# Kernel optimization log

Measured on AMD Instinct MI355X. Metric: run time of the kernel, lower is better.

The kernel has to match this reference:

```python
import jax, jax.numpy as jnp
import numpy as np

B, N, K = 32, 4096, 8          # batch, num input features (64x64 map), num slots
HID, D, DM = 256, 256, 512     # hid_dim, slot_dim, mlp_hid_dim
ITERS = 3
TEMP = 1.0
EPS = 1e-8
SCALE = D ** -0.5              # (slot_dim // num_heads) ** -0.5, heads=1


def layer_norm(x, g, b):
    m = jnp.mean(x, axis=-1, keepdims=True)
    v = jnp.mean((x - m) ** 2, axis=-1, keepdims=True)
    return (x - m) * jax.lax.rsqrt(v + 1e-5) * g + b


def setup_inputs() -> dict:
    key = jax.random.key(0)
    ks = jax.random.split(key, 20)
    s = 0.02
    inp = {
        "inputs": jax.random.normal(ks[0], (B, N, HID), jnp.float32),
        "noise": jax.random.normal(ks[1], (B, K, D), jnp.float32),
        "slots_mu": jax.random.normal(ks[2], (1, 1, D), jnp.float32),
        "slots_sigma": jnp.abs(jax.random.normal(ks[3], (1, 1, D), jnp.float32)),
        "ln_in_g": jnp.ones((HID,), jnp.float32),
        "ln_in_b": jnp.zeros((HID,), jnp.float32),
        "ln_slots_g": jnp.ones((D,), jnp.float32),
        "ln_slots_b": jnp.zeros((D,), jnp.float32),
        "ln_mlp_g": jnp.ones((D,), jnp.float32),
        "ln_mlp_b": jnp.zeros((D,), jnp.float32),
        # Linear weights stored [in, out]
        "Wq": jax.random.normal(ks[4], (D, D), jnp.float32) * s,
        "bq": jnp.zeros((D,), jnp.float32),
        "Wk": jax.random.normal(ks[5], (HID, D), jnp.float32) * s,
        "bk": jnp.zeros((D,), jnp.float32),
        "Wv": jax.random.normal(ks[6], (HID, D), jnp.float32) * s,
        "bv": jnp.zeros((D,), jnp.float32),
        # GRUCell params (torch layout transposed to [in, 3D])
        "W_ih": jax.random.normal(ks[7], (D, 3 * D), jnp.float32) * s,
        "W_hh": jax.random.normal(ks[8], (D, 3 * D), jnp.float32) * s,
        "b_ih": jnp.zeros((3 * D,), jnp.float32),
        "b_hh": jnp.zeros((3 * D,), jnp.float32),
        # residual MLP
        "W1": jax.random.normal(ks[9], (D, DM), jnp.float32) * s,
        "b1": jnp.zeros((DM,), jnp.float32),
        "W2": jax.random.normal(ks[10], (DM, D), jnp.float32) * s,
        "b2": jnp.zeros((D,), jnp.float32),
    }
    return inp


def reference(inputs, noise, slots_mu, slots_sigma,
              ln_in_g, ln_in_b, ln_slots_g, ln_slots_b, ln_mlp_g, ln_mlp_b,
              Wq, bq, Wk, bk, Wv, bv,
              W_ih, W_hh, b_ih, b_hh,
              W1, b1, W2, b2):
    x = layer_norm(inputs, ln_in_g, ln_in_b)            # [B,N,HID]
    k = x @ Wk + bk                                     # [B,N,D]
    v = x @ Wv + bv                                     # [B,N,D]

    slots = slots_mu + slots_sigma * noise              # [B,K,D]

    for _ in range(ITERS):
        slots_prev = slots
        s = layer_norm(slots, ln_slots_g, ln_slots_b)
        q = s @ Wq + bq                                  # [B,K,D]
        dots = jnp.einsum('bkd,bnd->bkn', q, k) * SCALE / TEMP
        attn = jax.nn.softmax(dots, axis=1)              # inverted: over slot axis
        attn = attn + EPS
        attn = attn / jnp.sum(attn, axis=2, keepdims=True)  # weighted mean over keys
        updates = jnp.einsum('bkn,bnd->bkd', attn, v)    # [B,K,D]

        # GRUCell on flattened (B*K, D)
        xg = updates.reshape(-1, D)
        h = slots_prev.reshape(-1, D)
        gi = xg @ W_ih + b_ih
        gh = h @ W_hh + b_hh
        i_r, i_z, i_n = jnp.split(gi, 3, axis=-1)
        h_r, h_z, h_n = jnp.split(gh, 3, axis=-1)
        r = jax.nn.sigmoid(i_r + h_r)
        z = jax.nn.sigmoid(i_z + h_z)
        n = jnp.tanh(i_n + r * h_n)
        h = (1.0 - z) * n + z * h
        slots = h.reshape(B, K, D)

        # residual MLP
        m = layer_norm(slots, ln_mlp_g, ln_mlp_b)
        slots = slots + (jax.nn.relu(m @ W1 + b1) @ W2 + b2)

    return slots
```

## Files before the change

kernel.cpp:

```cpp
#include <hip/hip_runtime.h>
#include <hip/hip_bf16.h>

#define NB 32
#define NPOS 4096
#define NSLOT 8
#define HIDD 256
#define DDIM 256
#define SCALE_F 0.0625f
#define EPS_F 1e-8f
#define NCHUNK 32
#define CPOS 128
#define TPOS 32

typedef __attribute__((ext_vector_type(4))) float f32x4;
typedef __attribute__((ext_vector_type(8))) short s16x8;
typedef __attribute__((ext_vector_type(2))) unsigned int u32x2;
typedef _Float16 h16x2 __attribute__((ext_vector_type(2)));

__device__ __forceinline__ unsigned short f2bf(float f) {
    unsigned int x = __float_as_uint(f);
    x = (x + 0x7fffu + ((x >> 16) & 1u)) >> 16;
    return (unsigned short)x;
}
__device__ __forceinline__ unsigned short f2h(float f) {
    _Float16 h = (_Float16)f;
    return __builtin_bit_cast(unsigned short, h);
}
__device__ __forceinline__ h16x2 u2h(unsigned u) { return __builtin_bit_cast(h16x2, u); }
__device__ __forceinline__ h16x2 mkh(float a0, float a1) {
    h16x2 r; r[0] = (_Float16)a0; r[1] = (_Float16)a1; return r;
}
__device__ __forceinline__ void dot4(f32x4& acc, uint4 wv, h16x2 av) {
    acc[0] = __builtin_amdgcn_fdot2(av, u2h(wv.x), acc[0], false);
    acc[1] = __builtin_amdgcn_fdot2(av, u2h(wv.y), acc[1], false);
    acc[2] = __builtin_amdgcn_fdot2(av, u2h(wv.z), acc[2], false);
    acc[3] = __builtin_amdgcn_fdot2(av, u2h(wv.w), acc[3], false);
}

__global__ __launch_bounds__(256) void k_ln_in(
        const float* __restrict__ x, const float* __restrict__ g,
        const float* __restrict__ b, unsigned short* __restrict__ lnx) {
    int lane = threadIdx.x & 63;
    int wave = threadIdx.x >> 6;
    long row = (long)blockIdx.x * 4 + wave;
    const float4* xr = (const float4*)(x + row * 256);
    float4 v = xr[lane];
    float s = v.x + v.y + v.z + v.w;
    float sq = v.x * v.x + v.y * v.y + v.z * v.z + v.w * v.w;
    #pragma unroll
    for (int m = 32; m; m >>= 1) { s += __shfl_xor(s, m); sq += __shfl_xor(sq, m); }
    float mean = s * 0.00390625f;
    float rstd = rsqrtf(sq * 0.00390625f - mean * mean + 1e-5f);
    const float4 gg = ((const float4*)g)[lane];
    const float4 bb = ((const float4*)b)[lane];
    ushort4 o;
    o.x = f2bf((v.x - mean) * rstd * gg.x + bb.x);
    o.y = f2bf((v.y - mean) * rstd * gg.y + bb.y);
    o.z = f2bf((v.z - mean) * rstd * gg.z + bb.z);
    o.w = f2bf((v.w - mean) * rstd * gg.w + bb.w);
    ((ushort4*)(lnx + row * 256))[lane] = o;
}

__device__ __forceinline__ unsigned packrowh(const float* __restrict__ W, int hp, int N, int c) {
    return (unsigned)f2h(W[(2*hp)*N + c]) | ((unsigned)f2h(W[(2*hp+1)*N + c]) << 16);
}

__global__ __launch_bounds__(256) void k_prep(
        const float* __restrict__ Wq, const float* __restrict__ Wk,
        const float* __restrict__ Wv, const float* __restrict__ Wih,
        const float* __restrict__ Whh, const float* __restrict__ W1,
        const float* __restrict__ W2,
        unsigned* __restrict__ WqP, unsigned* __restrict__ WkTP,
        unsigned* __restrict__ WvP, unsigned* __restrict__ WihP,
        unsigned* __restrict__ WhhP, unsigned* __restrict__ W1P,
        unsigned* __restrict__ W2P) {
    int i = blockIdx.x * 256 + threadIdx.x;
    if (i < 32768) {
        int hp = i >> 8, c = i & 255;
        WqP[i] = packrowh(Wq, hp, 256, c);
        WvP[i] = packrowh(Wv, hp, 256, c);
        WkTP[i] = (unsigned)f2h(Wk[c*256 + 2*hp]) | ((unsigned)f2h(Wk[c*256 + 2*hp + 1]) << 16);
    }
    if (i < 65536) {
        int hp1 = i >> 9, c1 = i & 511;
        W1P[i] = packrowh(W1, hp1, 512, c1);
        int hp2 = i >> 8, c2 = i & 255;
        W2P[i] = packrowh(W2, hp2, 256, c2);
    }
    if (i < 98304) {
        int hp = i / 768, c = i % 768;
        WihP[i] = packrowh(Wih, hp, 768, c);
        WhhP[i] = packrowh(Whh, hp, 768, c);
    }
}

__device__ __forceinline__ void qk_tail(
        float v0, float v1, int b, int s0,
        const float* __restrict__ lng, const float* __restrict__ lnb,
        const float* __restrict__ Wq, const float* __restrict__ bq,
        const float* __restrict__ Wk, const float* __restrict__ bk,
        unsigned short* __restrict__ qkg, float* __restrict__ qbkg,
        float (*sh)[256], float (*red)[4]) {
    int c = threadIdx.x;
    float s_0 = v0, q_0 = v0 * v0, s_1 = v1, q_1 = v1 * v1;
    #pragma unroll
    for (int m = 32; m; m >>= 1) {
        s_0 += __shfl_xor(s_0, m); q_0 += __shfl_xor(q_0, m);
        s_1 += __shfl_xor(s_1, m); q_1 += __shfl_xor(q_1, m);
    }
    if ((c & 63) == 0) { int w = c >> 6; red[w][0]=s_0; red[w][1]=q_0; red[w][2]=s_1; red[w][3]=q_1; }
    __syncthreads();
    float S0 = red[0][0]+red[1][0]+red[2][0]+red[3][0];
    float Q0 = red[0][1]+red[1][1]+red[2][1]+red[3][1];
    float S1 = red[0][2]+red[1][2]+red[2][2]+red[3][2];
    float Q1 = red[0][3]+red[1][3]+red[2][3]+red[3][3];
    float m0 = S0 * 0.00390625f, r0 = rsqrtf(Q0 * 0.00390625f - m0*m0 + 1e-5f);
    float m1 = S1 * 0.00390625f, r1 = rsqrtf(Q1 * 0.00390625f - m1*m1 + 1e-5f);
    float gc = lng[c], bc = lnb[c];
    sh[0][c] = (v0 - m0) * r0 * gc + bc;
    sh[1][c] = (v1 - m1) * r1 * gc + bc;
    __syncthreads();
    float qa0 = bq[c], qa1 = qa0;
    for (int h = 0; h < 256; h += 4) {
        float w0 = Wq[(h+0)*256+c], w1 = Wq[(h+1)*256+c];
        float w2 = Wq[(h+2)*256+c], w3 = Wq[(h+3)*256+c];
        float4 x0 = *(const float4*)&sh[0][h], x1 = *(const float4*)&sh[1][h];
        qa0 += x0.x*w0 + x0.y*w1 + x0.z*w2 + x0.w*w3;
        qa1 += x1.x*w0 + x1.y*w1 + x1.z*w2 + x1.w*w3;
    }
    __syncthreads();
    sh[0][c] = qa0; sh[1][c] = qa1;
    float bkc = bk[c];
    float p0 = qa0 * bkc, p1 = qa1 * bkc;
    #pragma unroll
    for (int m = 32; m; m >>= 1) { p0 += __shfl_xor(p0, m); p1 += __shfl_xor(p1, m); }
    __syncthreads();
    if ((c & 63) == 0) { int w = c >> 6; red[w][0] = p0; red[w][1] = p1; }
    __syncthreads();
    if (c < 2) qbkg[b*8 + s0 + c] = SCALE_F * (red[0][c]+red[1][c]+red[2][c]+red[3][c]);
    float k0 = 0.f, k1 = 0.f;
    const float* wkr = Wk + (long)c * 256;
    for (int d = 0; d < 256; d += 4) {
        float4 wk4 = *(const float4*)&wkr[d];
        float4 x0 = *(const float4*)&sh[0][d], x1 = *(const float4*)&sh[1][d];
        k0 += x0.x*wk4.x + x0.y*wk4.y + x0.z*wk4.z + x0.w*wk4.w;
        k1 += x1.x*wk4.x + x1.y*wk4.y + x1.z*wk4.z + x1.w*wk4.w;
    }
    qkg[(b*8 + s0    )*256 + c] = f2bf(SCALE_F * k0);
    qkg[(b*8 + s0 + 1)*256 + c] = f2bf(SCALE_F * k1);
}

__global__ __launch_bounds__(256) void k_init(
        const float* __restrict__ noise, const float* __restrict__ mu,
        const float* __restrict__ sig, const float* __restrict__ lng,
        const float* __restrict__ lnb, const float* __restrict__ Wq,
        const float* __restrict__ bq, const float* __restrict__ Wk,
        const float* __restrict__ bk, float* __restrict__ slots,
        unsigned short* __restrict__ qkg, float* __restrict__ qbkg) {
    __shared__ float sh[2][256];
    __shared__ float red[4][4];
    int b = blockIdx.x >> 2, rp = blockIdx.x & 3;
    int s0 = rp * 2, r0 = b * 8 + s0;
    int c = threadIdx.x;
    float v0 = mu[c] + sig[c] * noise[r0*256 + c];
    float v1 = mu[c] + sig[c] * noise[(r0+1)*256 + c];
    slots[r0*256 + c] = v0;
    slots[(r0+1)*256 + c] = v1;
    qk_tail(v0, v1, b, s0, lng, lnb, Wq, bq, Wk, bk, qkg, qbkg, sh, red);
}

__global__ __launch_bounds__(128) void k_stream(
        const unsigned short* __restrict__ lnx, const unsigned short* __restrict__ qk,
        const float* __restrict__ qbk, float* __restrict__ Upart,
        float* __restrict__ dpart) {
    __shared__ unsigned short xt[TPOS * 256];
    __shared__ float Ured[8 * 256];
    __shared__ float dred[8];
    int b = blockIdx.x >> 5, ch = blockIdx.x & 31;
    int t = threadIdx.x;
    int l = t & 63, w = t >> 6;
    for (int i = t; i < 2048; i += 128) Ured[i] = 0.f;
    if (t < 8) dred[t] = 0.f;
    int slot = l & 15, g = l >> 4;
    s16x8 qkf[8];
    float qbkv = 0.f;
    if (slot < 8) {
        const unsigned short* qrow = qk + (b*8 + slot) * 256;
        #pragma unroll
        for (int hk = 0; hk < 8; hk++)
            qkf[hk] = *(const s16x8*)(qrow + hk*32 + 8*g);
        qbkv = qbk[b*8 + slot];
    } else {
        #pragma unroll
        for (int hk = 0; hk < 8; hk++) qkf[hk] = (s16x8)0;
    }
    f32x4 uacc[16];
    #pragma unroll
    for (int i = 0; i < 16; i++) uacc[i] = (f32x4)0.f;
    float dreg = 0.f;
    int gbase = (b * NPOS + ch * CPOS) * 256;
    int pw = w * 16;
    __syncthreads();
    for (int tile = 0; tile < 4; tile++) {
        #pragma unroll
        for (int i = 0; i < 8; i++) {
            int c = t + 128 * i;
            int p = c >> 5, hc = c & 31;
            int4 v = *(const int4*)(lnx + gbase + (tile*TPOS + p)*256 + hc*8);
            *(int4*)&xt[p*256 + ((hc ^ (p & 15)) << 3)] = v;
        }
        __syncthreads();
        f32x4 acc = (f32x4)0.f;
        {
            int prow = pw + (l & 15);
            const unsigned short* xrow = &xt[prow * 256];
            int sw = prow & 15;
            #pragma unroll
            for (int hk = 0; hk < 8; hk++) {
                s16x8 a = *(const s16x8*)(xrow + (((hk*4 + g) ^ sw) << 3));
                acc = __builtin_amdgcn_mfma_f32_16x16x32_bf16(a, qkf[hk], acc, 0, 0, 0);
            }
        }
        float at[4];
        #pragma unroll
        for (int r = 0; r < 4; r++) {
            float v = acc[r] + qbkv;
            float m = v;
            m = fmaxf(m, __shfl_xor(m, 1));
            m = fmaxf(m, __shfl_xor(m, 2));
            m = fmaxf(m, __shfl_xor(m, 4));
            float e = __expf(v - m);
            float sum = e;
            sum += __shfl_xor(sum, 1);
            sum += __shfl_xor(sum, 2);
            sum += __shfl_xor(sum, 4);
            float a = e / sum;
            at[r] = a;
            dreg += a;
        }
        u32x2 a2;
        a2.x = (unsigned)f2bf(at[0]) | ((unsigned)f2bf(at[1]) << 16);
        a2.y = (unsigned)f2bf(at[2]) | ((unsigned)f2bf(at[3]) << 16);
        int p0 = pw + 4 * g;
        int hl = l & 7;
        #pragma unroll
        for (int hc = 0; hc < 16; hc++) {
            int hcol = hc * 2 + ((l & 15) >> 3);
            unsigned e0 = xt[(p0+0)*256 + ((hcol ^ ((p0+0) & 15)) << 3) + hl];
            unsigned e1 = xt[(p0+1)*256 + ((hcol ^ ((p0+1) & 15)) << 3) + hl];
            unsigned e2 = xt[(p0+2)*256 + ((hcol ^ ((p0+2) & 15)) << 3) + hl];
            unsigned e3 = xt[(p0+3)*256 + ((hcol ^ ((p0+3) & 15)) << 3) + hl];
            u32x2 b2;
            b2.x = e0 | (e1 << 16);
            b2.y = e2 | (e3 << 16);
            asm volatile("v_mfma_f32_16x16x16_bf16 %0, %1, %2, %0"
                         : "+v"(uacc[hc]) : "v"(a2), "v"(b2));
        }
        __syncthreads();
    }
    if (g < 2) {
        #pragma unroll
        for (int hc = 0; hc < 16; hc++) {
            int h = hc * 16 + (l & 15);
            #pragma unroll
            for (int r = 0; r < 4; r++)
                atomicAdd(&Ured[(4*g + r)*256 + h], uacc[hc][r]);
        }
    }
    dreg += __shfl_xor(dreg, 16);
    dreg += __shfl_xor(dreg, 32);
    if (slot < 8 && g == 0) atomicAdd(&dred[slot], dreg);
    __syncthreads();
    float* up = Upart + (long)(b * NCHUNK + ch) * 2048;
    for (int i = t; i < 2048; i += 128) up[i] = Ured[i];
    if (t < 8) dpart[(b * NCHUNK + ch) * 8 + t] = dred[t];
}

__device__ __forceinline__ float ln1024(float v, int c, const float* __restrict__ g,
                                        const float* __restrict__ b, float (*red)[2]) {
    float s1 = v, s2 = v * v;
    #pragma unroll
    for (int m = 32; m; m >>= 1) { s1 += __shfl_xor(s1, m); s2 += __shfl_xor(s2, m); }
    int w = threadIdx.x >> 6;
    if ((threadIdx.x & 63) == 0) { red[w][0] = s1; red[w][1] = s2; }
    __syncthreads();
    float S = 0.f, Q = 0.f;
    #pragma unroll
    for (int i = 0; i < 16; i++) { S += red[i][0]; Q += red[i][1]; }
    float mean = S * (1.f/1024.f);
    float rstd = rsqrtf(Q * (1.f/1024.f) - mean*mean + 1e-5f);
    __syncthreads();
    return (v - mean) * rstd * g[c] + b[c];
}

__global__ __launch_bounds__(1024) void k_post(
        const float* __restrict__ Upart, const float* __restrict__ dpart,
        const unsigned* __restrict__ WvP, const float* __restrict__ bv,
        const unsigned* __restrict__ WihP, const unsigned* __restrict__ WhhP,
        const float* __restrict__ bih, const float* __restrict__ bhh,
        const float* __restrict__ lnmg, const float* __restrict__ lnmb,
        const unsigned* __restrict__ W1P, const float* __restrict__ b1,
        const unsigned* __restrict__ W2P, const float* __restrict__ b2,
        const float* __restrict__ lnsg, const float* __restrict__ lnsb,
        const unsigned* __restrict__ WqP, const float* __restrict__ bq,
        const unsigned* __restrict__ WkTP, const float* __restrict__ bk,
        float* __restrict__ slots, unsigned short* __restrict__ qkg,
        float* __restrict__ qbkg, float* __restrict__ outp, int last) {
    __shared__ union {
        float PG[2][8][768];
        struct { float P16[16][256]; float H2[8][512]; } s;
    } sm;
    __shared__ float A[256], B[256], G2[2][768], H[512];
    __shared__ float red[16][2];
    __shared__ float scal[1];
    int r = blockIdx.x, b = r >> 3, s = r & 7;
    int t = threadIdx.x, c = t & 255, q = t >> 8;
    int cg = t & 63, kg16 = t >> 6;
    {
        float u = 0.f;
        const float* ub = Upart + (long)b * NCHUNK * 2048 + s * 256 + c;
        #pragma unroll
        for (int i = 0; i < 8; i++) u += ub[(q * 8 + i) * 2048];
        sm.s.P16[q][c] = u;
        if (q == 1) B[c] = slots[r * 256 + c];
        if (t < 32) {
            float dv = dpart[(b * NCHUNK + t) * 8 + s];
            #pragma unroll
            for (int m = 16; m; m >>= 1) dv += __shfl_xor(dv, m);
            if (t == 0) scal[0] = dv;
        }
    }
    __syncthreads();
    float dn = 1.f / (scal[0] + (float)NPOS * EPS_F);
    if (q == 0) A[c] = sm.s.P16[0][c] + sm.s.P16[1][c] + sm.s.P16[2][c] + sm.s.P16[3][c];
    __syncthreads();
    {
        f32x4 acc = (f32x4)0.f;
        const uint4* wp = (const uint4*)(WvP + kg16 * 8 * 256 + 4 * cg);
        #pragma unroll
        for (int i = 0; i < 8; i++) {
            uint4 wv = wp[i * 64];
            dot4(acc, wv, mkh(A[2*(kg16*8+i)], A[2*(kg16*8+i)+1]));
        }
        *(f32x4*)&sm.s.P16[kg16][4*cg] = acc;
    }
    __syncthreads();
    float updtmp;
    {
        float ss = 0.f;
        #pragma unroll
        for (int k = 0; k < 16; k++) ss += sm.s.P16[k][c];
        updtmp = ss * dn + bv[c];
    }
    __syncthreads();
    if (q == 0) A[c] = updtmp;
    __syncthreads();
    {
        int h = t >> 9;
        int kg = (t >> 6) & 7;
        const float* src = h ? B : A;
        const unsigned* W = h ? WhhP : WihP;
        f32x4 ar = (f32x4)0.f, az = (f32x4)0.f, an = (f32x4)0.f;
        #pragma unroll 4
        for (int i = 0; i < 16; i++) {
            int hp = kg * 16 + i;
            h16x2 av = mkh(src[2*hp], src[2*hp+1]);
            uint4 w0 = *(const uint4*)(W + hp*768 + 4*cg);
            uint4 w1 = *(const uint4*)(W + hp*768 + 256 + 4*cg);
            uint4 w2 = *(const uint4*)(W + hp*768 + 512 + 4*cg);
            dot4(ar, w0, av);
            dot4(az, w1, av);
            dot4(an, w2, av);
        }
        *(f32x4*)&sm.PG[h][kg][4*cg]       = ar;
        *(f32x4*)&sm.PG[h][kg][256 + 4*cg] = az;
        *(f32x4*)&sm.PG[h][kg][512 + 4*cg] = an;
    }
    __syncthreads();
    for (int idx = t; idx < 1536; idx += 1024) {
        int h = idx / 768, cc = idx - h * 768;
        float ss = 0.f;
        #pragma unroll
        for (int k = 0; k < 8; k++) ss += sm.PG[h][k][cc];
        G2[h][cc] = ss;
    }
    __syncthreads();
    float spc = B[c];
    float gir = bih[c]     + G2[0][c];
    float giz = bih[c+256] + G2[0][c+256];
    float gin = bih[c+512] + G2[0][c+512];
    float ghr = bhh[c]     + G2[1][c];
    float ghz = bhh[c+256] + G2[1][c+256];
    float ghn = bhh[c+512] + G2[1][c+512];
    float rg = 1.f/(1.f + __expf(-(gir+ghr)));
    float zg = 1.f/(1.f + __expf(-(giz+ghz)));
    float ng = tanhf(gin + rg*ghn);
    float hnew = (1.f - zg)*ng + zg*spc;
    float mmc = ln1024(hnew, c, lnmg, lnmb, red);
    if (q == 0) A[c] = mmc;
    __syncthreads();
    {
        int kg = t >> 7, cg1 = t & 127;
        f32x4 acc = (f32x4)0.f;
        const uint4* wp = (const uint4*)(W1P + kg * 16 * 512 + 4 * cg1);
        #pragma unroll 4
        for (int i = 0; i < 16; i++) {
            uint4 wv = wp[i * 128];
            dot4(acc, wv, mkh(A[2*(kg*16+i)], A[2*(kg*16+i)+1]));
        }
        *(f32x4*)&sm.s.H2[kg][4*cg1] = acc;
    }
    __syncthreads();
    if (t < 512) {
        float ss = b1[t];
        #pragma unroll
        for (int k = 0; k < 8; k++) ss += sm.s.H2[k][t];
        H[t] = fmaxf(ss, 0.f);
    }
    __syncthreads();
    {
        f32x4 acc = (f32x4)0.f;
        const uint4* wp = (const uint4*)(W2P + kg16 * 16 * 256 + 4 * cg);
        #pragma unroll 4
        for (int i = 0; i < 16; i++) {
            uint4 wv = wp[i * 64];
            dot4(acc, wv, mkh(H[2*(kg16*16+i)], H[2*(kg16*16+i)+1]));
        }
        *(f32x4*)&sm.s.P16[kg16][4*cg] = acc;
    }
    __syncthreads();
    float outc;
    {
        float ss = 0.f;
        #pragma unroll
        for (int k = 0; k < 16; k++) ss += sm.s.P16[k][c];
        outc = hnew + ss + b2[c];
    }
    if (t < 256) {
        slots[r*256 + c] = outc;
        if (last) outp[r*256 + c] = outc;
    }
    if (last) return;
    __syncthreads();
    float sc = ln1024(outc, c, lnsg, lnsb, red);
    if (q == 0) A[c] = sc;
    __syncthreads();
    {
        f32x4 acc = (f32x4)0.f;
        const uint4* wp = (const uint4*)(WqP + kg16 * 8 * 256 + 4 * cg);
        #pragma unroll
        for (int i = 0; i < 8; i++) {
            uint4 wv = wp[i * 64];
            dot4(acc, wv, mkh(A[2*(kg16*8+i)], A[2*(kg16*8+i)+1]));
        }
        *(f32x4*)&sm.s.P16[kg16][4*cg] = acc;
    }
    __syncthreads();
    float qc;
    {
        float ss = 0.f;
        #pragma unroll
        for (int k = 0; k < 16; k++) ss += sm.s.P16[k][c];
        qc = ss + bq[c];
    }
    {
        float v = qc * bk[c];
        #pragma unroll
        for (int m = 32; m; m >>= 1) v += __shfl_xor(v, m);
        int w = t >> 6;
        if ((t & 63) == 0) red[w][0] = v;
        __syncthreads();
        if (t == 0) {
            float S = 0.f;
            #pragma unroll
            for (int i = 0; i < 16; i++) S += red[i][0];
            qbkg[r] = SCALE_F * 0.25f * S;
        }
        __syncthreads();
    }
    if (q == 0) A[c] = qc;
    __syncthreads();
    {
        f32x4 acc = (f32x4)0.f;
        const uint4* wp = (const uint4*)(WkTP + kg16 * 8 * 256 + 4 * cg);
        #pragma unroll
        for (int i = 0; i < 8; i++) {
            uint4 wv = wp[i * 64];
            dot4(acc, wv, mkh(A[2*(kg16*8+i)], A[2*(kg16*8+i)+1]));
        }
        *(f32x4*)&sm.s.P16[kg16][4*cg] = acc;
    }
    __syncthreads();
    if (t < 256) {
        float ss = 0.f;
        #pragma unroll
        for (int k = 0; k < 16; k++) ss += sm.s.P16[k][c];
        qkg[r*256 + c] = f2bf(SCALE_F * ss);
    }
}

extern "C" void kernel_launch(void* const* d_in, const int* in_sizes, int n_in,
                              void* d_out, int out_size, void* d_ws, size_t ws_size,
                              hipStream_t stream) {
    const float* inputs = (const float*)d_in[0];
    const float* noise  = (const float*)d_in[1];
    const float* mu     = (const float*)d_in[2];
    const float* sig    = (const float*)d_in[3];
    const float* lnig   = (const float*)d_in[4];
    const float* lnib   = (const float*)d_in[5];
    const float* lnsg   = (const float*)d_in[6];
    const float* lnsb   = (const float*)d_in[7];
    const float* lnmg   = (const float*)d_in[8];
    const float* lnmb   = (const float*)d_in[9];
    const float* Wq     = (const float*)d_in[10];
    const float* bq     = (const float*)d_in[11];
    const float* Wk     = (const float*)d_in[12];
    const float* bk     = (const float*)d_in[13];
    const float* Wv     = (const float*)d_in[14];
    const float* bv     = (const float*)d_in[15];
    const float* Wih    = (const float*)d_in[16];
    const float* Whh    = (const float*)d_in[17];
    const float* bih    = (const float*)d_in[18];
    const float* bhh    = (const float*)d_in[19];
    const float* W1     = (const float*)d_in[20];
    const float* b1     = (const float*)d_in[21];
    const float* W2     = (const float*)d_in[22];
    const float* b2     = (const float*)d_in[23];

    char* ws = (char*)d_ws;
    unsigned short* lnx = (unsigned short*)ws;
    size_t off = (size_t)NB * NPOS * HIDD * 2;
    unsigned short* qkb = (unsigned short*)(ws + off); off += (size_t)NB*NSLOT*HIDD*2;
    float* qbk   = (float*)(ws + off); off += (size_t)NB*NSLOT*4;
    float* Upart = (float*)(ws + off); off += (size_t)NB*NCHUNK*NSLOT*HIDD*4;
    float* dpart = (float*)(ws + off); off += (size_t)NB*NCHUNK*NSLOT*4;
    float* slots = (float*)(ws + off); off += (size_t)NB*NSLOT*DDIM*4;
    unsigned* WqP  = (unsigned*)(ws + off); off += 32768u*4;
    unsigned* WkTP = (unsigned*)(ws + off); off += 32768u*4;
    unsigned* WvP  = (unsigned*)(ws + off); off += 32768u*4;
    unsigned* WihP = (unsigned*)(ws + off); off += 98304u*4;
    unsigned* WhhP = (unsigned*)(ws + off); off += 98304u*4;
    unsigned* W1P  = (unsigned*)(ws + off); off += 65536u*4;
    unsigned* W2P  = (unsigned*)(ws + off); off += 65536u*4;

    k_prep<<<384, 256, 0, stream>>>(Wq, Wk, Wv, Wih, Whh, W1, W2,
                                    WqP, WkTP, WvP, WihP, WhhP, W1P, W2P);
    k_ln_in<<<NB*NPOS/4, 256, 0, stream>>>(inputs, lnig, lnib, lnx);
    k_init<<<NB*4, 256, 0, stream>>>(noise, mu, sig, lnsg, lnsb, Wq, bq, Wk, bk,
                                     slots, qkb, qbk);
    for (int it = 0; it < 3; it++) {
        k_stream<<<NB*NCHUNK, 128, 0, stream>>>(lnx, qkb, qbk, Upart, dpart);
        k_post<<<NB*NSLOT, 1024, 0, stream>>>(Upart, dpart,
                                              WvP, bv, WihP, WhhP, bih, bhh,
                                              lnmg, lnmb, W1P, b1, W2P, b2,
                                              lnsg, lnsb, WqP, bq, WkTP, bk,
                                              slots, qkb, qbk, (float*)d_out,
                                              it == 2 ? 1 : 0);
    }
}
```

Baseline: 233.0 us.

## Pre-fold Wv into W_ih and Wq into Wk to shorten per-slot chains

Precomputes the fused matrices Wv·W_ih and Wq·Wk^T, plus folded bias vectors, in the prep kernel. This removes two dependent matvec stages and several block barriers from each k_post iteration, leaving one matvec for the GRU input gates and one for the query-key vector. It also makes the input-layernorm load nontemporal. The cost is a heavier one-time prep kernel with naive fp32 matrix products, and the folded weights are rounded to fp16, which may change numerics slightly.

New measurement: 289.9 us. 1.24x slower.

```diff
diff --git a/kernel.cpp b/kernel.cpp
--- a/kernel.cpp
+++ b/kernel.cpp
@@ -26,6 +26,9 @@
     _Float16 h = (_Float16)f;
     return __builtin_bit_cast(unsigned short, h);
 }
+__device__ __forceinline__ unsigned pack2h(float a, float b) {
+    return (unsigned)f2h(a) | ((unsigned)f2h(b) << 16);
+}
 __device__ __forceinline__ h16x2 u2h(unsigned u) { return __builtin_bit_cast(h16x2, u); }
 __device__ __forceinline__ h16x2 mkh(float a0, float a1) {
     h16x2 r; r[0] = (_Float16)a0; r[1] = (_Float16)a1; return r;
@@ -35,6 +38,16 @@
     acc[1] = __builtin_amdgcn_fdot2(av, u2h(wv.y), acc[1], false);
     acc[2] = __builtin_amdgcn_fdot2(av, u2h(wv.z), acc[2], false);
     acc[3] = __builtin_amdgcn_fdot2(av, u2h(wv.w), acc[3], false);
+}
+__device__ __forceinline__ float blkred(float v, float* red4) {
+    #pragma unroll
+    for (int m = 32; m; m >>= 1) v += __shfl_xor(v, m);
+    int w = threadIdx.x >> 6;
+    if ((threadIdx.x & 63) == 0) red4[w] = v;
+    __syncthreads();
+    float s = red4[0] + red4[1] + red4[2] + red4[3];
+    __syncthreads();
+    return s;
 }
 
 __global__ __launch_bounds__(256) void k_ln_in(
@@ -43,10 +56,9 @@
     int lane = threadIdx.x & 63;
     int wave = threadIdx.x >> 6;
     long row = (long)blockIdx.x * 4 + wave;
-    const float4* xr = (const float4*)(x + row * 256);
-    float4 v = xr[lane];
-    float s = v.x + v.y + v.z + v.w;
-    float sq = v.x * v.x + v.y * v.y + v.z * v.z + v.w * v.w;
+    f32x4 v = __builtin_nontemporal_load((const f32x4*)(x + row * 256) + lane);
+    float s = v[0] + v[1] + v[2] + v[3];
+    float sq = v[0]*v[0] + v[1]*v[1] + v[2]*v[2] + v[3]*v[3];
     #pragma unroll
     for (int m = 32; m; m >>= 1) { s += __shfl_xor(s, m); sq += __shfl_xor(sq, m); }
     float mean = s * 0.00390625f;
@@ -54,55 +66,111 @@
     const float4 gg = ((const float4*)g)[lane];
     const float4 bb = ((const float4*)b)[lane];
     ushort4 o;
-    o.x = f2bf((v.x - mean) * rstd * gg.x + bb.x);
-    o.y = f2bf((v.y - mean) * rstd * gg.y + bb.y);
-    o.z = f2bf((v.z - mean) * rstd * gg.z + bb.z);
-    o.w = f2bf((v.w - mean) * rstd * gg.w + bb.w);
+    o.x = f2bf((v[0] - mean) * rstd * gg.x + bb.x);
+    o.y = f2bf((v[1] - mean) * rstd * gg.y + bb.y);
+    o.z = f2bf((v[2] - mean) * rstd * gg.z + bb.z);
+    o.w = f2bf((v[3] - mean) * rstd * gg.w + bb.w);
     ((ushort4*)(lnx + row * 256))[lane] = o;
 }
 
 __device__ __forceinline__ unsigned packrowh(const float* __restrict__ W, int hp, int N, int c) {
-    return (unsigned)f2h(W[(2*hp)*N + c]) | ((unsigned)f2h(W[(2*hp+1)*N + c]) << 16);
+    return pack2h(W[(2*hp)*N + c], W[(2*hp+1)*N + c]);
 }
 
 __global__ __launch_bounds__(256) void k_prep(
         const float* __restrict__ Wq, const float* __restrict__ Wk,
+        const float* __restrict__ bq, const float* __restrict__ bk,
         const float* __restrict__ Wv, const float* __restrict__ Wih,
         const float* __restrict__ Whh, const float* __restrict__ W1,
-        const float* __restrict__ W2,
-        unsigned* __restrict__ WqP, unsigned* __restrict__ WkTP,
-        unsigned* __restrict__ WvP, unsigned* __restrict__ WihP,
+        const float* __restrict__ W2, const float* __restrict__ bih,
+        const float* __restrict__ bv,
         unsigned* __restrict__ WhhP, unsigned* __restrict__ W1P,
-        unsigned* __restrict__ W2P) {
-    int i = blockIdx.x * 256 + threadIdx.x;
-    if (i < 32768) {
-        int hp = i >> 8, c = i & 255;
-        WqP[i] = packrowh(Wq, hp, 256, c);
-        WvP[i] = packrowh(Wv, hp, 256, c);
-        WkTP[i] = (unsigned)f2h(Wk[c*256 + 2*hp]) | ((unsigned)f2h(Wk[c*256 + 2*hp + 1]) << 16);
-    }
-    if (i < 65536) {
-        int hp1 = i >> 9, c1 = i & 511;
-        W1P[i] = packrowh(W1, hp1, 512, c1);
-        int hp2 = i >> 8, c2 = i & 255;
-        W2P[i] = packrowh(W2, hp2, 256, c2);
-    }
-    if (i < 98304) {
-        int hp = i / 768, c = i % 768;
-        WihP[i] = packrowh(Wih, hp, 768, c);
-        WhhP[i] = packrowh(Whh, hp, 768, c);
+        unsigned* __restrict__ W2P, unsigned* __restrict__ M1P,
+        unsigned* __restrict__ M_ihP, float* __restrict__ bihP,
+        float* __restrict__ v1, float* __restrict__ w2, float* __restrict__ sc2) {
+    int t = threadIdx.x;
+    if (blockIdx.x < 384) {
+        int i = blockIdx.x * 256 + t;
+        if (i < 65536) {
+            int hp1 = i >> 9, c1 = i & 511;
+            W1P[i] = packrowh(W1, hp1, 512, c1);
+            int hp2 = i >> 8, c2 = i & 255;
+            W2P[i] = packrowh(W2, hp2, 256, c2);
+        }
+        if (i < 98304) {
+            int hp = i / 768, c = i % 768;
+            WhhP[i] = packrowh(Whh, hp, 768, c);
+        }
+        return;
+    }
+    if (blockIdx.x < 512) {
+        __shared__ float wq0[256], wq1[256], bqL[256];
+        __shared__ float red4[4];
+        int e2 = blockIdx.x - 384;
+        wq0[t] = Wq[(2*e2)*256 + t];
+        wq1[t] = Wq[(2*e2+1)*256 + t];
+        bqL[t] = bq[t];
+        __syncthreads();
+        const float4* wkr = (const float4*)(Wk + (long)t * 256);
+        float a0 = 0.f, a1 = 0.f;
+        for (int d = 0; d < 64; d++) {
+            float4 k4 = wkr[d];
+            a0 += wq0[4*d]*k4.x + wq0[4*d+1]*k4.y + wq0[4*d+2]*k4.z + wq0[4*d+3]*k4.w;
+            a1 += wq1[4*d]*k4.x + wq1[4*d+1]*k4.y + wq1[4*d+2]*k4.z + wq1[4*d+3]*k4.w;
+        }
+        M1P[e2*256 + t] = pack2h(a0, a1);
+        float p0 = blkred(wq0[t] * bk[t], red4);
+        float p1 = blkred(wq1[t] * bk[t], red4);
+        if (t == 0) { w2[2*e2] = p0; w2[2*e2+1] = p1; }
+        if (e2 == 0) {
+            float av = 0.f;
+            for (int d = 0; d < 64; d++) {
+                float4 k4 = wkr[d];
+                av += bqL[4*d]*k4.x + bqL[4*d+1]*k4.y + bqL[4*d+2]*k4.z + bqL[4*d+3]*k4.w;
+            }
+            v1[t] = av;
+            float p2 = blkred(bqL[t] * bk[t], red4);
+            if (t == 0) sc2[0] = p2;
+        }
+        return;
+    }
+    if (blockIdx.x < 544) {
+        __shared__ float wvr[8][256];
+        int bb = blockIdx.x - 512;
+        #pragma unroll
+        for (int r = 0; r < 8; r++) wvr[r][t] = Wv[(8*bb + r)*256 + t];
+        __syncthreads();
+        for (int jj = 0; jj < 3; jj++) {
+            int j = t + jj*256;
+            float acc[8] = {0.f,0.f,0.f,0.f,0.f,0.f,0.f,0.f};
+            for (int c = 0; c < 256; c++) {
+                float w = Wih[c*768 + j];
+                #pragma unroll
+                for (int r = 0; r < 8; r++) acc[r] += wvr[r][c] * w;
+            }
+            #pragma unroll
+            for (int p = 0; p < 4; p++)
+                M_ihP[(4*bb + p)*768 + j] = pack2h(acc[2*p], acc[2*p+1]);
+        }
+        return;
+    }
+    for (int jj = 0; jj < 3; jj++) {
+        int j = t + jj*256;
+        float a = bih[j];
+        for (int c = 0; c < 256; c++) a += bv[c] * Wih[c*768 + j];
+        bihP[j] = a;
     }
 }
 
 __device__ __forceinline__ void qk_tail(
-        float v0, float v1, int b, int s0,
+        float v0, float v1_, int b, int s0,
         const float* __restrict__ lng, const float* __restrict__ lnb,
         const float* __restrict__ Wq, const float* __restrict__ bq,
         const float* __restrict__ Wk, const float* __restrict__ bk,
         unsigned short* __restrict__ qkg, float* __restrict__ qbkg,
         float (*sh)[256], float (*red)[4]) {
     int c = threadIdx.x;
-    float s_0 = v0, q_0 = v0 * v0, s_1 = v1, q_1 = v1 * v1;
+    float s_0 = v0, q_0 = v0 * v0, s_1 = v1_, q_1 = v1_ * v1_;
     #pragma unroll
     for (int m = 32; m; m >>= 1) {
         s_0 += __shfl_xor(s_0, m); q_0 += __shfl_xor(q_0, m);
@@ -118,15 +186,15 @@
     float m1 = S1 * 0.00390625f, r1 = rsqrtf(Q1 * 0.00390625f - m1*m1 + 1e-5f);
     float gc = lng[c], bc = lnb[c];
     sh[0][c] = (v0 - m0) * r0 * gc + bc;
-    sh[1][c] = (v1 - m1) * r1 * gc + bc;
+    sh[1][c] = (v1_ - m1) * r1 * gc + bc;
     __syncthreads();
     float qa0 = bq[c], qa1 = qa0;
     for (int h = 0; h < 256; h += 4) {
         float w0 = Wq[(h+0)*256+c], w1 = Wq[(h+1)*256+c];
-        float w2 = Wq[(h+2)*256+c], w3 = Wq[(h+3)*256+c];
+        float w2_ = Wq[(h+2)*256+c], w3 = Wq[(h+3)*256+c];
         float4 x0 = *(const float4*)&sh[0][h], x1 = *(const float4*)&sh[1][h];
-        qa0 += x0.x*w0 + x0.y*w1 + x0.z*w2 + x0.w*w3;
-        qa1 += x1.x*w0 + x1.y*w1 + x1.z*w2 + x1.w*w3;
+        qa0 += x0.x*w0 + x0.y*w1 + x0.z*w2_ + x0.w*w3;
+        qa1 += x1.x*w0 + x1.y*w1 + x1.z*w2_ + x1.w*w3;
     }
     __syncthreads();
     sh[0][c] = qa0; sh[1][c] = qa1;
@@ -295,15 +363,14 @@
 
 __global__ __launch_bounds__(1024) void k_post(
         const float* __restrict__ Upart, const float* __restrict__ dpart,
-        const unsigned* __restrict__ WvP, const float* __restrict__ bv,
-        const unsigned* __restrict__ WihP, const unsigned* __restrict__ WhhP,
-        const float* __restrict__ bih, const float* __restrict__ bhh,
+        const unsigned* __restrict__ M_ihP, const unsigned* __restrict__ WhhP,
+        const float* __restrict__ bihP, const float* __restrict__ bhh,
         const float* __restrict__ lnmg, const float* __restrict__ lnmb,
         const unsigned* __restrict__ W1P, const float* __restrict__ b1,
         const unsigned* __restrict__ W2P, const float* __restrict__ b2,
         const float* __restrict__ lnsg, const float* __restrict__ lnsb,
-        const unsigned* __restrict__ WqP, const float* __restrict__ bq,
-        const unsigned* __restrict__ WkTP, const float* __restrict__ bk,
+        const unsigned* __restrict__ M1P, const float* __restrict__ v1g,
+        const float* __restrict__ w2g, const float* __restrict__ sc2g,
         float* __restrict__ slots, unsigned short* __restrict__ qkg,
         float* __restrict__ qbkg, float* __restrict__ outp, int last) {
     __shared__ union {
@@ -332,34 +399,14 @@
     }
     __syncthreads();
     float dn = 1.f / (scal[0] + (float)NPOS * EPS_F);
-    if (q == 0) A[c] = sm.s.P16[0][c] + sm.s.P16[1][c] + sm.s.P16[2][c] + sm.s.P16[3][c];
-    __syncthreads();
-    {
-        f32x4 acc = (f32x4)0.f;
-        const uint4* wp = (const uint4*)(WvP + kg16 * 8 * 256 + 4 * cg);
-        #pragma unroll
-        for (int i = 0; i < 8; i++) {
-            uint4 wv = wp[i * 64];
-            dot4(acc, wv, mkh(A[2*(kg16*8+i)], A[2*(kg16*8+i)+1]));
-        }
-        *(f32x4*)&sm.s.P16[kg16][4*cg] = acc;
-    }
-    __syncthreads();
-    float updtmp;
-    {
-        float ss = 0.f;
-        #pragma unroll
-        for (int k = 0; k < 16; k++) ss += sm.s.P16[k][c];
-        updtmp = ss * dn + bv[c];
-    }
-    __syncthreads();
-    if (q == 0) A[c] = updtmp;
+    if (q == 0)
+        A[c] = (sm.s.P16[0][c] + sm.s.P16[1][c] + sm.s.P16[2][c] + sm.s.P16[3][c]) * dn;
     __syncthreads();
     {
         int h = t >> 9;
         int kg = (t >> 6) & 7;
         const float* src = h ? B : A;
-        const unsigned* W = h ? WhhP : WihP;
+        const unsigned* W = h ? WhhP : M_ihP;
         f32x4 ar = (f32x4)0.f, az = (f32x4)0.f, an = (f32x4)0.f;
         #pragma unroll 4
         for (int i = 0; i < 16; i++) {
@@ -386,12 +433,12 @@
     }
     __syncthreads();
     float spc = B[c];
-    float gir = bih[c]     + G2[0][c];
-    float giz = bih[c+256] + G2[0][c+256];
-    float gin = bih[c+512] + G2[0][c+512];
-    float ghr = bhh[c]     + G2[1][c];
-    float ghz = bhh[c+256] + G2[1][c+256];
-    float ghn = bhh[c+512] + G2[1][c+512];
+    float gir = bihP[c]     + G2[0][c];
+    float giz = bihP[c+256] + G2[0][c+256];
+    float gin = bihP[c+512] + G2[0][c+512];
+    float ghr = bhh[c]      + G2[1][c];
+    float ghz = bhh[c+256]  + G2[1][c+256];
+    float ghn = bhh[c+512]  + G2[1][c+512];
     float rg = 1.f/(1.f + __expf(-(gir+ghr)));
     float zg = 1.f/(1.f + __expf(-(giz+ghz)));
     float ng = tanhf(gin + rg*ghn);
@@ -444,10 +491,23 @@
     __syncthreads();
     float sc = ln1024(outc, c, lnsg, lnsb, red);
     if (q == 0) A[c] = sc;
-    __syncthreads();
+    {
+        float v = sc * w2g[c];
+        #pragma unroll
+        for (int m = 32; m; m >>= 1) v += __shfl_xor(v, m);
+        int w = t >> 6;
+        if ((t & 63) == 0) red[w][0] = v;
+    }
+    __syncthreads();
+    if (t == 0) {
+        float S = 0.f;
+        #pragma unroll
+        for (int i = 0; i < 16; i++) S += red[i][0];
+        qbkg[r] = SCALE_F * (0.25f * S + sc2g[0]);
+    }
     {
         f32x4 acc = (f32x4)0.f;
-        const uint4* wp = (const uint4*)(WqP + kg16 * 8 * 256 + 4 * cg);
+        const uint4* wp = (const uint4*)(M1P + kg16 * 8 * 256 + 4 * cg);
         #pragma unroll
         for (int i = 0; i < 8; i++) {
             uint4 wv = wp[i * 64];
@@ -456,46 +516,11 @@
         *(f32x4*)&sm.s.P16[kg16][4*cg] = acc;
     }
     __syncthreads();
-    float qc;
-    {
-        float ss = 0.f;
-        #pragma unroll
-        for (int k = 0; k < 16; k++) ss += sm.s.P16[k][c];
-        qc = ss + bq[c];
-    }
-    {
-        float v = qc * bk[c];
-        #pragma unroll
-        for (int m = 32; m; m >>= 1) v += __shfl_xor(v, m);
-        int w = t >> 6;
-        if ((t & 63) == 0) red[w][0] = v;
-        __syncthreads();
-        if (t == 0) {
-            float S = 0.f;
-            #pragma unroll
-            for (int i = 0; i < 16; i++) S += red[i][0];
-            qbkg[r] = SCALE_F * 0.25f * S;
-        }
-        __syncthreads();
-    }
-    if (q == 0) A[c] = qc;
-    __syncthreads();
-    {
-        f32x4 acc = (f32x4)0.f;
-        const uint4* wp = (const uint4*)(WkTP + kg16 * 8 * 256 + 4 * cg);
-        #pragma unroll
-        for (int i = 0; i < 8; i++) {
-            uint4 wv = wp[i * 64];
-            dot4(acc, wv, mkh(A[2*(kg16*8+i)], A[2*(kg16*8+i)+1]));
-        }
-        *(f32x4*)&sm.s.P16[kg16][4*cg] = acc;
-    }
-    __syncthreads();
     if (t < 256) {
         float ss = 0.f;
         #pragma unroll
         for (int k = 0; k < 16; k++) ss += sm.s.P16[k][c];
-        qkg[r*256 + c] = f2bf(SCALE_F * ss);
+        qkg[r*256 + c] = f2bf(SCALE_F * (ss + v1g[c]));
     }
 }
 
@@ -535,25 +560,27 @@
     float* Upart = (float*)(ws + off); off += (size_t)NB*NCHUNK*NSLOT*HIDD*4;
     float* dpart = (float*)(ws + off); off += (size_t)NB*NCHUNK*NSLOT*4;
     float* slots = (float*)(ws + off); off += (size_t)NB*NSLOT*DDIM*4;
-    unsigned* WqP  = (unsigned*)(ws + off); off += 32768u*4;
-    unsigned* WkTP = (unsigned*)(ws + off); off += 32768u*4;
-    unsigned* WvP  = (unsigned*)(ws + off); off += 32768u*4;
-    unsigned* WihP = (unsigned*)(ws + off); off += 98304u*4;
-    unsigned* WhhP = (unsigned*)(ws + off); off += 98304u*4;
-    unsigned* W1P  = (unsigned*)(ws + off); off += 65536u*4;
-    unsigned* W2P  = (unsigned*)(ws + off); off += 65536u*4;
-
-    k_prep<<<384, 256, 0, stream>>>(Wq, Wk, Wv, Wih, Whh, W1, W2,
-                                    WqP, WkTP, WvP, WihP, WhhP, W1P, W2P);
+    unsigned* WhhP  = (unsigned*)(ws + off); off += 98304u*4;
+    unsigned* W1P   = (unsigned*)(ws + off); off += 65536u*4;
+    unsigned* W2P   = (unsigned*)(ws + off); off += 65536u*4;
+    unsigned* M1P   = (unsigned*)(ws + off); off += 32768u*4;
+    unsigned* M_ihP = (unsigned*)(ws + off); off += 98304u*4;
+    float* bihP = (float*)(ws + off); off += 768*4;
+    float* v1   = (float*)(ws + off); off += 256*4;
+    float* w2   = (float*)(ws + off); off += 256*4;
+    float* sc2  = (float*)(ws + off); off += 64;
+
+    k_prep<<<545, 256, 0, stream>>>(Wq, Wk, bq, bk, Wv, Wih, Whh, W1, W2, bih, bv,
+                                    WhhP, W1P, W2P, M1P, M_ihP, bihP, v1, w2, sc2);
     k_ln_in<<<NB*NPOS/4, 256, 0, stream>>>(inputs, lnig, lnib, lnx);
     k_init<<<NB*4, 256, 0, stream>>>(noise, mu, sig, lnsg, lnsb, Wq, bq, Wk, bk,
                                      slots, qkb, qbk);
     for (int it = 0; it < 3; it++) {
         k_stream<<<NB*NCHUNK, 128, 0, stream>>>(lnx, qkb, qbk, Upart, dpart);
         k_post<<<NB*NSLOT, 1024, 0, stream>>>(Upart, dpart,
-                                              WvP, bv, WihP, WhhP, bih, bhh,
+                                              M_ihP, WhhP, bihP, bhh,
                                               lnmg, lnmb, W1P, b1, W2P, b2,
-                                              lnsg, lnsb, WqP, bq, WkTP, bk,
+                                              lnsg, lnsb, M1P, v1, w2, sc2,
                                               slots, qkb, qbk, (float*)d_out,
                                               it == 2 ? 1 : 0);
     }
```
